# Kernel tuning notes

Hardware: AMD Instinct MI355X
Metric: run time of the kernel (lower is better)

Reference implementation:

```python
import jax, jax.numpy as jnp
import numpy as np

RADIUS = 0.2
NSAMPLE = 32
GROUPS = 4
EPS = 1e-5


def group_norm(x, gamma, beta):
    # x: [B, C, *spatial]; normalize per (batch, group) over channels-in-group + spatial
    B, C = x.shape[0], x.shape[1]
    rest = x.shape[2:]
    xr = x.reshape(B, GROUPS, -1)
    mean = xr.mean(-1, keepdims=True)
    var = xr.var(-1, keepdims=True)
    xr = (xr - mean) * jax.lax.rsqrt(var + EPS)
    x = xr.reshape((B, C) + rest)
    bshape = (1, C) + (1,) * len(rest)
    return x * gamma.reshape(bshape) + beta.reshape(bshape)


def ball_query(pos_t):
    # pos_t: [B, N, 3] -> idx [B, N, NSAMPLE] (query points == all points)
    N = pos_t.shape[1]
    sq = jnp.sum(pos_t * pos_t, axis=-1)  # [B, N]
    d = sq[:, :, None] + sq[:, None, :] - 2.0 * jnp.einsum('bnc,bmc->bnm', pos_t, pos_t)
    ar = jnp.arange(N, dtype=jnp.int32)
    gi = jnp.where(d > RADIUS * RADIUS, N, ar[None, None, :])  # [B, S, N]
    gi = jnp.sort(gi, axis=-1)[:, :, :NSAMPLE]  # ascending in-ball indices first
    first = gi[:, :, :1]
    gi = jnp.where(gi == N, first, gi)  # pad with first neighbor
    return gi


def setup_inputs() -> dict:
    key = jax.random.key(0)
    ks = jax.random.split(key, 6)
    B, C, N = 2, 64, 4096
    M = 4 * C  # mid channels
    return {
        'x': jax.random.normal(ks[0], (B, C, N), jnp.float32),
        'pos': jax.random.uniform(ks[1], (B, 3, N), jnp.float32),
        'w1': jax.random.normal(ks[2], (M, C), jnp.float32) * 0.05,
        'b1': jnp.zeros((M,), jnp.float32),
        'g1': jnp.ones((M,), jnp.float32),
        'be1': jnp.zeros((M,), jnp.float32),
        'wd': 1.0 + jax.random.normal(ks[3], (M,), jnp.float32) * 0.05,
        'gd': jnp.ones((M,), jnp.float32),
        'bed': jnp.zeros((M,), jnp.float32),
        'w2': jax.random.normal(ks[4], (C, M), jnp.float32) * 0.05,
        'b2': jnp.zeros((C,), jnp.float32),
        'g2': jnp.ones((C,), jnp.float32),
        'be2': jnp.zeros((C,), jnp.float32),
    }


def reference(x, pos, w1, b1, g1, be1, wd, gd, bed, w2, b2, g2, be2):
    # x: [B, C, N], pos: [B, 3, N]
    pos_t = jnp.transpose(pos, (0, 2, 1))  # [B, N, 3]
    idx = ball_query(pos_t)  # [B, N, K]

    # conv1 (1x1) -> GroupNorm -> GELU
    h = jnp.einsum('mc,bcn->bmn', w1, x) + b1[None, :, None]
    h = jax.nn.gelu(group_norm(h, g1, be1), approximate=False)  # [B, M, N]

    # gather neighbors: feats [B, N, M] indexed by idx [B, N, K]
    feats = jnp.transpose(h, (0, 2, 1))
    grouped = jax.vmap(lambda f, i: f[i])(feats, idx)  # [B, N, K, M]
    grouped = jnp.transpose(grouped, (0, 3, 1, 2))  # [B, M, N, K]

    # depthwise 1x1 conv (per-channel scale, no bias) -> GroupNorm -> max-pool over K -> GELU
    grouped = grouped * wd[None, :, None, None]
    grouped = group_norm(grouped, gd, bed)
    h2 = jax.nn.gelu(jnp.max(grouped, axis=-1), approximate=False)  # [B, M, N]

    # conv2 (1x1) -> GroupNorm -> residual
    out = jnp.einsum('cm,bmn->bcn', w2, h2) + b2[None, :, None]
    out = group_norm(out, g2, be2)
    return out + x
```

## Files before the change

### kernel.cpp

```cpp
#include <hip/hip_runtime.h>
#include <hip/hip_fp16.h>
#include <math.h>

#define BB 2
#define CC 64
#define NN 4096
#define MM 256
#define KK 32
#define GG 4
#define EPSF 1e-5f

__device__ __forceinline__ float gelu_exact(float x) {
    return 0.5f * x * (1.0f + erff(x * 0.70710678118654752f));
}

__device__ __forceinline__ unsigned pkmax(unsigned a, unsigned b) {
    unsigned d;
    asm volatile("v_pk_max_f16 %0, %1, %2" : "=v"(d) : "v"(a), "v"(b));
    return d;
}
__device__ __forceinline__ unsigned pkmin(unsigned a, unsigned b) {
    unsigned d;
    asm volatile("v_pk_min_f16 %0, %1, %2" : "=v"(d) : "v"(a), "v"(b));
    return d;
}
__device__ __forceinline__ unsigned selpair(unsigned mx, unsigned mn, float g0, float g1) {
    unsigned lo = (g0 >= 0.f) ? (mx & 0x0000FFFFu) : (mn & 0x0000FFFFu);
    unsigned hi = (g1 >= 0.f) ? (mx & 0xFFFF0000u) : (mn & 0xFFFF0000u);
    return lo | hi;
}
__device__ __forceinline__ float bcast_lane(float v, int lane) {
    return __int_as_float(__builtin_amdgcn_readlane(__float_as_int(v), lane));
}

__global__ void k_mlp1(const float* __restrict__ x, const float* __restrict__ w1,
                       const float* __restrict__ b1, float* __restrict__ h,
                       float2* __restrict__ Mp) {
    __shared__ float xs[64 * 128];
    __shared__ float w1t[64 * 32];
    __shared__ float r1[4], r2[4];

    int bx = blockIdx.x;
    int nt = bx & 31, mt = (bx >> 5) & 7, b = bx >> 8;
    int n0 = nt * 128, m0 = mt * 32;
    int t = threadIdx.x;

    {
        int nq = t & 31, ch = t >> 5;
        #pragma unroll
        for (int p = 0; p < 8; p++) {
            int c = p * 8 + ch;
            float4 v = *(const float4*)&x[((size_t)(b * CC + c)) * NN + n0 + nq * 4];
            *(float4*)&xs[c * 128 + nq * 4] = v;
        }
    }
    {
        #pragma unroll
        for (int p = 0; p < 2; p++) {
            int idx = p * 256 + t;
            int m = idx >> 4, cq = idx & 15;
            float4 v = *(const float4*)&w1[(m0 + m) * CC + cq * 4];
            w1t[(cq * 4 + 0) * 32 + m] = v.x;
            w1t[(cq * 4 + 1) * 32 + m] = v.y;
            w1t[(cq * 4 + 2) * 32 + m] = v.z;
            w1t[(cq * 4 + 3) * 32 + m] = v.w;
        }
    }
    __syncthreads();

    int nq = t & 31;
    int mseg = t >> 5;
    float o[4][4];
    #pragma unroll
    for (int i = 0; i < 4; i++)
        #pragma unroll
        for (int j = 0; j < 4; j++) o[i][j] = 0.f;

    for (int c = 0; c < 64; c++) {
        float4 xv = *(float4*)&xs[c * 128 + nq * 4];
        float4 wv = *(float4*)&w1t[c * 32 + mseg * 4];
        o[0][0] = fmaf(wv.x, xv.x, o[0][0]); o[0][1] = fmaf(wv.x, xv.y, o[0][1]);
        o[0][2] = fmaf(wv.x, xv.z, o[0][2]); o[0][3] = fmaf(wv.x, xv.w, o[0][3]);
        o[1][0] = fmaf(wv.y, xv.x, o[1][0]); o[1][1] = fmaf(wv.y, xv.y, o[1][1]);
        o[1][2] = fmaf(wv.y, xv.z, o[1][2]); o[1][3] = fmaf(wv.y, xv.w, o[1][3]);
        o[2][0] = fmaf(wv.z, xv.x, o[2][0]); o[2][1] = fmaf(wv.z, xv.y, o[2][1]);
        o[2][2] = fmaf(wv.z, xv.z, o[2][2]); o[2][3] = fmaf(wv.z, xv.w, o[2][3]);
        o[3][0] = fmaf(wv.w, xv.x, o[3][0]); o[3][1] = fmaf(wv.w, xv.y, o[3][1]);
        o[3][2] = fmaf(wv.w, xv.z, o[3][2]); o[3][3] = fmaf(wv.w, xv.w, o[3][3]);
    }

    float s1 = 0.f, s2 = 0.f;
    #pragma unroll
    for (int mi = 0; mi < 4; mi++) {
        int m = m0 + mseg * 4 + mi;
        float bv = b1[m];
        float4 r;
        r.x = o[mi][0] + bv; r.y = o[mi][1] + bv;
        r.z = o[mi][2] + bv; r.w = o[mi][3] + bv;
        *(float4*)&h[((size_t)(b * MM + m)) * NN + n0 + nq * 4] = r;
        s1 += r.x + r.y + r.z + r.w;
        s2 = fmaf(r.x, r.x, s2); s2 = fmaf(r.y, r.y, s2);
        s2 = fmaf(r.z, r.z, s2); s2 = fmaf(r.w, r.w, s2);
    }
    for (int off = 32; off; off >>= 1) {
        s1 += __shfl_down(s1, off, 64);
        s2 += __shfl_down(s2, off, 64);
    }
    int w = t >> 6, l = t & 63;
    if (l == 0) { r1[w] = s1; r2[w] = s2; }
    __syncthreads();
    if (t == 0) {
        Mp[bx] = make_float2(r1[0] + r1[1] + r1[2] + r1[3],
                             r2[0] + r2[1] + r2[2] + r2[3]);
    }
}

__global__ void k_gn1t_ballq(const float* __restrict__ h, const float* __restrict__ g1,
                             const float* __restrict__ be1, const float* __restrict__ wd,
                             const float2* __restrict__ Mp, __half* __restrict__ pH,
                             float* __restrict__ R,
                             const float* __restrict__ pos, int* __restrict__ idx) {
    __shared__ float tile[64 * 65];
    __shared__ float mv[2];
    int t = threadIdx.x;

    if (blockIdx.x < 512) {
        int id = blockIdx.x;
        int n0 = (id & 63) * 64;
        int g  = (id >> 6) & 3;
        int b  = id >> 8;
        int m0 = g * 64;

        if (t < 64) {
            float2 p2 = Mp[b * 256 + g * 64 + t];
            float s1 = p2.x, s2 = p2.y;
            for (int off = 32; off; off >>= 1) {
                s1 += __shfl_down(s1, off, 64);
                s2 += __shfl_down(s2, off, 64);
            }
            if (t == 0) {
                const double cnt = 64.0 * 4096.0;
                double md = (double)s1 / cnt;
                double vd = (double)s2 / cnt - md * md;
                mv[0] = (float)md;
                mv[1] = rsqrtf((float)vd + EPSF);
            }
        }
        __syncthreads();
        float mean = mv[0], rstd = mv[1];

        int nq = t & 15, mr = t >> 4;
        #pragma unroll
        for (int pp = 0; pp < 4; pp++) {
            int row = pp * 16 + mr;
            int m = m0 + row;
            float a = rstd * g1[m];
            float cc2 = be1[m] - mean * a;
            float wdm = wd[m];
            float4 hv = *(const float4*)&h[((size_t)(b * MM + m)) * NN + n0 + nq * 4];
            tile[row * 65 + nq * 4 + 0] = gelu_exact(fmaf(hv.x, a, cc2)) * wdm;
            tile[row * 65 + nq * 4 + 1] = gelu_exact(fmaf(hv.y, a, cc2)) * wdm;
            tile[row * 65 + nq * 4 + 2] = gelu_exact(fmaf(hv.z, a, cc2)) * wdm;
            tile[row * 65 + nq * 4 + 3] = gelu_exact(fmaf(hv.w, a, cc2)) * wdm;
        }
        __syncthreads();
        #pragma unroll
        for (int pp = 0; pp < 4; pp++) {
            int id2 = pp * 256 + t;
            int nl = id2 >> 4, mq = id2 & 15;
            float a0 = tile[(mq * 4 + 0) * 65 + nl];
            float a1 = tile[(mq * 4 + 1) * 65 + nl];
            float a2 = tile[(mq * 4 + 2) * 65 + nl];
            float a3 = tile[(mq * 4 + 3) * 65 + nl];
            __half2 hA = __float22half2_rn(make_float2(a0, a1));
            __half2 hB = __float22half2_rn(make_float2(a2, a3));
            uint2 st8;
            st8.x = *(unsigned*)&hA; st8.y = *(unsigned*)&hB;
            *(uint2*)((char*)pH + ((((size_t)(b * NN) + n0 + nl)) << 9) + (m0 + mq * 4) * 2) = st8;
            float2 fa = __half22float2(hA);
            float2 fb = __half22float2(hB);
            float t1 = fa.x + fa.y + fb.x + fb.y;
            float t2 = fa.x * fa.x + fa.y * fa.y + fb.x * fb.x + fb.y * fb.y;
            #pragma unroll
            for (int off = 8; off; off >>= 1) {
                t1 += __shfl_down(t1, off, 16);
                t2 += __shfl_down(t2, off, 16);
            }
            if ((t & 15) == 0) {
                float* rr = &R[((size_t)(b * NN) + n0 + nl) * 8];
                rr[g]     = t1;
                rr[4 + g] = t2;
            }
        }
    } else {
        int bx = blockIdx.x - 512;
        int wid  = bx * 4 + (threadIdx.x >> 6);
        int lane = threadIdx.x & 63;
        int b = wid >> 12;
        int n = wid & 4095;
        const float* px = pos + b * 3 * NN;
        const float* py = px + NN;
        const float* pz = py + NN;
        float qx = px[n], qy = py[n], qz = pz[n];
        float qsq = qx*qx + qy*qy + qz*qz;
        int* row = idx + (b * NN + n) * KK;

        int found = 0;
        int first = -1;
        const float R2 = 0.04f;
        for (int m0 = 0; m0 < NN && found < KK; m0 += 64) {
            int m = m0 + lane;
            float ax = px[m], ay = py[m], az = pz[m];
            float msq = ax*ax + ay*ay + az*az;
            float dot = qx*ax + qy*ay + qz*az;
            float d = qsq + msq - 2.0f * dot;
            bool hit = !(d > R2);
            unsigned long long mask = __ballot(hit);
            if (first < 0 && mask) first = m0 + (__ffsll((long long)mask) - 1);
            unsigned long long lt = (lane == 0) ? 0ULL : (mask & ((1ULL << lane) - 1ULL));
            int posh = __popcll(lt);
            if (hit && (found + posh) < KK) row[found + posh] = m;
            found += __popcll(mask);
            if (found > KK) found = KK;
        }
        if (lane < KK && lane >= found) row[lane] = first;
    }
}

__global__ __launch_bounds__(256)
void k_qgather_gstats(const __half* __restrict__ pH, const int* __restrict__ idx,
                      const float* __restrict__ R, const float* __restrict__ gd,
                      __half* __restrict__ pselH, float* __restrict__ Gp) {
    __shared__ float sAcc[8][8];
    int t = threadIdx.x;

    if (blockIdx.x < 2048) {
        int w = t >> 6, l = t & 63;
        int gn = blockIdx.x * 4 + w;
        int b = gn >> 12;

        int hh = l >> 5, cl = l & 31;
        int myidx = idx[gn * KK + cl];
        const char* pb = (const char*)(pH + (size_t)b * NN * 256);
        int laneoff = cl * 16;

        unsigned vmax0 = 0xFC00FC00u, vmax1 = 0xFC00FC00u, vmax2 = 0xFC00FC00u, vmax3 = 0xFC00FC00u;
        unsigned vmin0 = 0x7C007C00u, vmin1 = 0x7C007C00u, vmin2 = 0x7C007C00u, vmin3 = 0x7C007C00u;

        #pragma unroll
        for (int k = 0; k < 16; k++) {
            int ja = __shfl(myidx, 2 * k, 64);
            int jb = __shfl(myidx, 2 * k + 1, 64);
            int j = hh ? jb : ja;
            uint4 raw = *(const uint4*)(pb + (((size_t)j) << 9) + laneoff);
            vmax0 = pkmax(vmax0, raw.x); vmin0 = pkmin(vmin0, raw.x);
            vmax1 = pkmax(vmax1, raw.y); vmin1 = pkmin(vmin1, raw.y);
            vmax2 = pkmax(vmax2, raw.z); vmin2 = pkmin(vmin2, raw.z);
            vmax3 = pkmax(vmax3, raw.w); vmin3 = pkmin(vmin3, raw.w);
        }
        vmax0 = pkmax(vmax0, (unsigned)__shfl_xor((int)vmax0, 32, 64));
        vmax1 = pkmax(vmax1, (unsigned)__shfl_xor((int)vmax1, 32, 64));
        vmax2 = pkmax(vmax2, (unsigned)__shfl_xor((int)vmax2, 32, 64));
        vmax3 = pkmax(vmax3, (unsigned)__shfl_xor((int)vmax3, 32, 64));
        vmin0 = pkmin(vmin0, (unsigned)__shfl_xor((int)vmin0, 32, 64));
        vmin1 = pkmin(vmin1, (unsigned)__shfl_xor((int)vmin1, 32, 64));
        vmin2 = pkmin(vmin2, (unsigned)__shfl_xor((int)vmin2, 32, 64));
        vmin3 = pkmin(vmin3, (unsigned)__shfl_xor((int)vmin3, 32, 64));

        if (hh == 0) {
            const float4* g4 = (const float4*)gd;
            float4 gA = g4[cl * 2], gB = g4[cl * 2 + 1];
            uint4 out;
            out.x = selpair(vmax0, vmin0, gA.x, gA.y);
            out.y = selpair(vmax1, vmin1, gA.z, gA.w);
            out.z = selpair(vmax2, vmin2, gB.x, gB.y);
            out.w = selpair(vmax3, vmin3, gB.z, gB.w);
            *(uint4*)((char*)pselH + (((size_t)gn) << 9) + laneoff) = out;
        }
    } else {
        int bid = blockIdx.x - 2048;
        int hw = t >> 5, cl = t & 31;
        int pbase = bid * 32;
        int b = pbase >> 12;
        float s[8];
        #pragma unroll
        for (int c = 0; c < 8; c++) s[c] = 0.f;
        #pragma unroll
        for (int it = 0; it < 4; it++) {
            int pt = pbase + it * 8 + hw;
            int j = idx[pt * KK + cl];
            const float* rr = &R[((size_t)(b * NN) + j) * 8];
            float4 ra = *(const float4*)rr;
            float4 rb = *(const float4*)(rr + 4);
            s[0] += ra.x; s[1] += ra.y; s[2] += ra.z; s[3] += ra.w;
            s[4] += rb.x; s[5] += rb.y; s[6] += rb.z; s[7] += rb.w;
        }
        #pragma unroll
        for (int off = 16; off; off >>= 1) {
            #pragma unroll
            for (int c = 0; c < 8; c++) s[c] += __shfl_down(s[c], off, 32);
        }
        if (cl == 0) {
            #pragma unroll
            for (int c = 0; c < 8; c++) sAcc[hw][c] = s[c];
        }
        __syncthreads();
        if (t < 8) {
            float v = 0.f;
            #pragma unroll
            for (int k = 0; k < 8; k++) v += sAcc[k][t];
            Gp[bid * 8 + t] = v;
        }
    }
}

__global__ __launch_bounds__(256, 4)
void k_mlp2(const __half* __restrict__ pselH, const float* __restrict__ Gp,
            const float* __restrict__ w2, const float* __restrict__ b2,
            const float* __restrict__ gd, const float* __restrict__ bed,
            float* __restrict__ oraw, float* __restrict__ Op) {
    __shared__ float w2s[64 * 257];
    __shared__ float sw[4][8];
    __shared__ float sA[4][4], sB[4][4];

    int t = threadIdx.x;
    int w = t >> 6, l = t & 63;
    int b  = blockIdx.x >> 7;
    int n0 = (blockIdx.x & 127) * 32 + w * 8;

    #pragma unroll
    for (int p = 0; p < 16; p++) {
        int i = p * 256 + t;
        int c = i >> 6, mq = i & 63;
        float4 v = ((const float4*)w2)[i];
        float* dst = &w2s[c * 257 + mq * 4];
        dst[0] = v.x; dst[1] = v.y; dst[2] = v.z; dst[3] = v.w;
    }

    {
        float s[8] = {0.f, 0.f, 0.f, 0.f, 0.f, 0.f, 0.f, 0.f};
        if (t < 128) {
            const float4* gp = (const float4*)(Gp + ((size_t)(b * 128 + t)) * 8);
            float4 ra = gp[0], rb = gp[1];
            s[0] = ra.x; s[1] = ra.y; s[2] = ra.z; s[3] = ra.w;
            s[4] = rb.x; s[5] = rb.y; s[6] = rb.z; s[7] = rb.w;
        }
        #pragma unroll
        for (int off = 32; off; off >>= 1) {
            #pragma unroll
            for (int c = 0; c < 8; c++) s[c] += __shfl_down(s[c], off, 64);
        }
        if (l == 0) {
            #pragma unroll
            for (int c = 0; c < 8; c++) sw[w][c] = s[c];
        }
    }
    __syncthreads();

    int g = l >> 4;
    double s1 = (double)sw[0][g] + sw[1][g] + sw[2][g] + sw[3][g];
    double s2 = (double)sw[0][4 + g] + sw[1][4 + g] + sw[2][4 + g] + sw[3][4 + g];
    const double cnt2 = 64.0 * 4096.0 * 32.0;
    double m_ = s1 / cnt2;
    double v_ = s2 / cnt2 - m_ * m_;
    float mean = (float)m_;
    float rstd = rsqrtf((float)v_ + EPSF);
    float4 gd4  = ((const float4*)gd)[l];
    float4 bed4 = ((const float4*)bed)[l];
    float ax = rstd * gd4.x, ay = rstd * gd4.y, az = rstd * gd4.z, aw = rstd * gd4.w;
    float cx = bed4.x - mean * ax, cy = bed4.y - mean * ay;
    float cz = bed4.z - mean * az, cw = bed4.w - mean * aw;

    float4 h2r[8];
    #pragma unroll
    for (int j = 0; j < 8; j++) {
        uint2 raw = *(const uint2*)((const char*)pselH +
                     ((((size_t)(b * NN)) + n0 + j) << 9) + l * 8);
        float2 fa = __half22float2(*(__half2*)&raw.x);
        float2 fb = __half22float2(*(__half2*)&raw.y);
        h2r[j].x = gelu_exact(fmaf(fa.x, ax, cx));
        h2r[j].y = gelu_exact(fmaf(fa.y, ay, cy));
        h2r[j].z = gelu_exact(fmaf(fb.x, az, cz));
        h2r[j].w = gelu_exact(fmaf(fb.y, aw, cw));
    }

    const float* w2l = &w2s[l * 257];
    float acc[8];
    #pragma unroll
    for (int j = 0; j < 8; j++) acc[j] = 0.f;

    #pragma unroll 8
    for (int mq = 0; mq < 64; mq++) {
        float w0  = w2l[4 * mq + 0];
        float w1_ = w2l[4 * mq + 1];
        float w2_ = w2l[4 * mq + 2];
        float w3_ = w2l[4 * mq + 3];
        #pragma unroll
        for (int j = 0; j < 8; j++) {
            acc[j] = fmaf(w0,  bcast_lane(h2r[j].x, mq), acc[j]);
            acc[j] = fmaf(w1_, bcast_lane(h2r[j].y, mq), acc[j]);
            acc[j] = fmaf(w2_, bcast_lane(h2r[j].z, mq), acc[j]);
            acc[j] = fmaf(w3_, bcast_lane(h2r[j].w, mq), acc[j]);
        }
    }

    float bias = b2[l];
    float so1 = 0.f, so2 = 0.f;
    #pragma unroll
    for (int j = 0; j < 8; j++) {
        acc[j] += bias;
        so1 += acc[j];
        so2 = fmaf(acc[j], acc[j], so2);
    }
    float* dst = &oraw[((size_t)(b * CC) + l) * NN + n0];
    *(float4*)&dst[0] = make_float4(acc[0], acc[1], acc[2], acc[3]);
    *(float4*)&dst[4] = make_float4(acc[4], acc[5], acc[6], acc[7]);

    so1 += __shfl_down(so1, 8, 16); so2 += __shfl_down(so2, 8, 16);
    so1 += __shfl_down(so1, 4, 16); so2 += __shfl_down(so2, 4, 16);
    so1 += __shfl_down(so1, 2, 16); so2 += __shfl_down(so2, 2, 16);
    so1 += __shfl_down(so1, 1, 16); so2 += __shfl_down(so2, 1, 16);
    if ((l & 15) == 0) { sA[w][l >> 4] = so1; sB[w][l >> 4] = so2; }
    __syncthreads();
    if (t < 8) {
        int is2 = t >> 2, gg = t & 3;
        float v = is2 ? (sB[0][gg] + sB[1][gg] + sB[2][gg] + sB[3][gg])
                      : (sA[0][gg] + sA[1][gg] + sA[2][gg] + sA[3][gg]);
        Op[blockIdx.x * 8 + t] = v;
    }
}

__global__ void k_final(const float* __restrict__ oraw, const float* __restrict__ x,
                        const float* __restrict__ g2, const float* __restrict__ be2,
                        const float* __restrict__ Op, float* __restrict__ out) {
    __shared__ float fw[4][8];
    int t = threadIdx.x;
    int i4 = blockIdx.x * 256 + t;
    int base = i4 * 4;
    int b = base >> 18;

    {
        float s[8] = {0.f, 0.f, 0.f, 0.f, 0.f, 0.f, 0.f, 0.f};
        if (t < 128) {
            const float4* rp = (const float4*)(Op + ((size_t)(b * 128 + t)) * 8);
            float4 ra = rp[0], rb = rp[1];
            s[0] = ra.x; s[1] = ra.y; s[2] = ra.z; s[3] = ra.w;
            s[4] = rb.x; s[5] = rb.y; s[6] = rb.z; s[7] = rb.w;
        }
        #pragma unroll
        for (int off = 32; off; off >>= 1) {
            #pragma unroll
            for (int c = 0; c < 8; c++) s[c] += __shfl_down(s[c], off, 64);
        }
        if ((t & 63) == 0) {
            #pragma unroll
            for (int c = 0; c < 8; c++) fw[t >> 6][c] = s[c];
        }
    }
    __syncthreads();

    int c = (base >> 12) & 63;
    int g = c >> 4;
    double s1 = (double)fw[0][g] + fw[1][g] + fw[2][g] + fw[3][g];
    double s2 = (double)fw[0][4 + g] + fw[1][4 + g] + fw[2][4 + g] + fw[3][4 + g];
    const double cnt = 16.0 * 4096.0;
    double mean_d = s1 / cnt;
    double var_d  = s2 / cnt - mean_d * mean_d;
    float mean = (float)mean_d;
    float rstd = rsqrtf((float)var_d + EPSF);
    float sc = rstd * g2[c];
    float ad = be2[c] - mean * sc;
    float4 o = ((const float4*)oraw)[i4];
    float4 xv = ((const float4*)x)[i4];
    float4 r;
    r.x = fmaf(o.x, sc, ad) + xv.x;
    r.y = fmaf(o.y, sc, ad) + xv.y;
    r.z = fmaf(o.z, sc, ad) + xv.z;
    r.w = fmaf(o.w, sc, ad) + xv.w;
    ((float4*)out)[i4] = r;
}

extern "C" void kernel_launch(void* const* d_in, const int* in_sizes, int n_in,
                              void* d_out, int out_size, void* d_ws, size_t ws_size,
                              hipStream_t stream) {
    const float* x   = (const float*)d_in[0];
    const float* pos = (const float*)d_in[1];
    const float* w1  = (const float*)d_in[2];
    const float* b1  = (const float*)d_in[3];
    const float* g1  = (const float*)d_in[4];
    const float* be1 = (const float*)d_in[5];
    const float* wd  = (const float*)d_in[6];
    const float* gd  = (const float*)d_in[7];
    const float* bed = (const float*)d_in[8];
    const float* w2  = (const float*)d_in[9];
    const float* b2  = (const float*)d_in[10];
    const float* g2  = (const float*)d_in[11];
    const float* be2 = (const float*)d_in[12];
    float* out = (float*)d_out;

    char* wsb = (char*)d_ws;
    float*  h     = (float*)wsb;
    __half* pH    = (__half*)(wsb + 8388608);
    __half* pselH = (__half*)(wsb + 12582912);
    float*  oraw  = (float*)(wsb + 16777216);
    int*    idx   = (int*)(wsb + 18874368);
    float*  R     = (float*)(wsb + 19922944);
    float2* Mp    = (float2*)(wsb + 20185088);
    float*  Gp    = (float*)(wsb + 20189184);
    float*  Op    = (float*)(wsb + 20197376);

    k_mlp1<<<512, 256, 0, stream>>>(x, w1, b1, h, Mp);
    k_gn1t_ballq<<<2560, 256, 0, stream>>>(h, g1, be1, wd, Mp, pH, R, pos, idx);
    k_qgather_gstats<<<2304, 256, 0, stream>>>(pH, idx, R, gd, pselH, Gp);
    k_mlp2<<<256, 256, 0, stream>>>(pselH, Gp, w2, b2, gd, bed, oraw, Op);
    k_final<<<512, 256, 0, stream>>>(oraw, x, g2, be2, Op, out);
}
```

Before: 148.9 us.

## Move ball query into mlp1 kernel and fuse final GN into mlp2 via grid barrier

```diff
diff --git a/kernel.cpp b/kernel.cpp
--- a/kernel.cpp
+++ b/kernel.cpp
@@ -33,164 +33,87 @@
     return __int_as_float(__builtin_amdgcn_readlane(__float_as_int(v), lane));
 }
 
-__global__ void k_mlp1(const float* __restrict__ x, const float* __restrict__ w1,
-                       const float* __restrict__ b1, float* __restrict__ h,
-                       float2* __restrict__ Mp) {
+__global__ void k_mlp1_ballq(const float* __restrict__ x, const float* __restrict__ w1,
+                             const float* __restrict__ b1, float* __restrict__ h,
+                             float2* __restrict__ Mp,
+                             const float* __restrict__ pos, int* __restrict__ idx) {
     __shared__ float xs[64 * 128];
     __shared__ float w1t[64 * 32];
     __shared__ float r1[4], r2[4];
-
-    int bx = blockIdx.x;
-    int nt = bx & 31, mt = (bx >> 5) & 7, b = bx >> 8;
-    int n0 = nt * 128, m0 = mt * 32;
     int t = threadIdx.x;
 
-    {
-        int nq = t & 31, ch = t >> 5;
-        #pragma unroll
-        for (int p = 0; p < 8; p++) {
-            int c = p * 8 + ch;
-            float4 v = *(const float4*)&x[((size_t)(b * CC + c)) * NN + n0 + nq * 4];
-            *(float4*)&xs[c * 128 + nq * 4] = v;
-        }
-    }
-    {
-        #pragma unroll
-        for (int p = 0; p < 2; p++) {
-            int idx = p * 256 + t;
-            int m = idx >> 4, cq = idx & 15;
-            float4 v = *(const float4*)&w1[(m0 + m) * CC + cq * 4];
-            w1t[(cq * 4 + 0) * 32 + m] = v.x;
-            w1t[(cq * 4 + 1) * 32 + m] = v.y;
-            w1t[(cq * 4 + 2) * 32 + m] = v.z;
-            w1t[(cq * 4 + 3) * 32 + m] = v.w;
-        }
-    }
-    __syncthreads();
-
-    int nq = t & 31;
-    int mseg = t >> 5;
-    float o[4][4];
-    #pragma unroll
-    for (int i = 0; i < 4; i++)
-        #pragma unroll
-        for (int j = 0; j < 4; j++) o[i][j] = 0.f;
-
-    for (int c = 0; c < 64; c++) {
-        float4 xv = *(float4*)&xs[c * 128 + nq * 4];
-        float4 wv = *(float4*)&w1t[c * 32 + mseg * 4];
-        o[0][0] = fmaf(wv.x, xv.x, o[0][0]); o[0][1] = fmaf(wv.x, xv.y, o[0][1]);
-        o[0][2] = fmaf(wv.x, xv.z, o[0][2]); o[0][3] = fmaf(wv.x, xv.w, o[0][3]);
-        o[1][0] = fmaf(wv.y, xv.x, o[1][0]); o[1][1] = fmaf(wv.y, xv.y, o[1][1]);
-        o[1][2] = fmaf(wv.y, xv.z, o[1][2]); o[1][3] = fmaf(wv.y, xv.w, o[1][3]);
-        o[2][0] = fmaf(wv.z, xv.x, o[2][0]); o[2][1] = fmaf(wv.z, xv.y, o[2][1]);
-        o[2][2] = fmaf(wv.z, xv.z, o[2][2]); o[2][3] = fmaf(wv.z, xv.w, o[2][3]);
-        o[3][0] = fmaf(wv.w, xv.x, o[3][0]); o[3][1] = fmaf(wv.w, xv.y, o[3][1]);
-        o[3][2] = fmaf(wv.w, xv.z, o[3][2]); o[3][3] = fmaf(wv.w, xv.w, o[3][3]);
-    }
-
-    float s1 = 0.f, s2 = 0.f;
-    #pragma unroll
-    for (int mi = 0; mi < 4; mi++) {
-        int m = m0 + mseg * 4 + mi;
-        float bv = b1[m];
-        float4 r;
-        r.x = o[mi][0] + bv; r.y = o[mi][1] + bv;
-        r.z = o[mi][2] + bv; r.w = o[mi][3] + bv;
-        *(float4*)&h[((size_t)(b * MM + m)) * NN + n0 + nq * 4] = r;
-        s1 += r.x + r.y + r.z + r.w;
-        s2 = fmaf(r.x, r.x, s2); s2 = fmaf(r.y, r.y, s2);
-        s2 = fmaf(r.z, r.z, s2); s2 = fmaf(r.w, r.w, s2);
-    }
-    for (int off = 32; off; off >>= 1) {
-        s1 += __shfl_down(s1, off, 64);
-        s2 += __shfl_down(s2, off, 64);
-    }
-    int w = t >> 6, l = t & 63;
-    if (l == 0) { r1[w] = s1; r2[w] = s2; }
-    __syncthreads();
-    if (t == 0) {
-        Mp[bx] = make_float2(r1[0] + r1[1] + r1[2] + r1[3],
-                             r2[0] + r2[1] + r2[2] + r2[3]);
-    }
-}
-
-__global__ void k_gn1t_ballq(const float* __restrict__ h, const float* __restrict__ g1,
-                             const float* __restrict__ be1, const float* __restrict__ wd,
-                             const float2* __restrict__ Mp, __half* __restrict__ pH,
-                             float* __restrict__ R,
-                             const float* __restrict__ pos, int* __restrict__ idx) {
-    __shared__ float tile[64 * 65];
-    __shared__ float mv[2];
-    int t = threadIdx.x;
-
     if (blockIdx.x < 512) {
-        int id = blockIdx.x;
-        int n0 = (id & 63) * 64;
-        int g  = (id >> 6) & 3;
-        int b  = id >> 8;
-        int m0 = g * 64;
-
-        if (t < 64) {
-            float2 p2 = Mp[b * 256 + g * 64 + t];
-            float s1 = p2.x, s2 = p2.y;
-            for (int off = 32; off; off >>= 1) {
-                s1 += __shfl_down(s1, off, 64);
-                s2 += __shfl_down(s2, off, 64);
+        int bx = blockIdx.x;
+        int nt = bx & 31, mt = (bx >> 5) & 7, b = bx >> 8;
+        int n0 = nt * 128, m0 = mt * 32;
+
+        {
+            int nq = t & 31, ch = t >> 5;
+            #pragma unroll
+            for (int p = 0; p < 8; p++) {
+                int c = p * 8 + ch;
+                float4 v = *(const float4*)&x[((size_t)(b * CC + c)) * NN + n0 + nq * 4];
+                *(float4*)&xs[c * 128 + nq * 4] = v;
             }
-            if (t == 0) {
-                const double cnt = 64.0 * 4096.0;
-                double md = (double)s1 / cnt;
-                double vd = (double)s2 / cnt - md * md;
-                mv[0] = (float)md;
-                mv[1] = rsqrtf((float)vd + EPSF);
+        }
+        {
+            #pragma unroll
+            for (int p = 0; p < 2; p++) {
+                int i = p * 256 + t;
+                int m = i >> 4, cq = i & 15;
+                float4 v = *(const float4*)&w1[(m0 + m) * CC + cq * 4];
+                w1t[(cq * 4 + 0) * 32 + m] = v.x;
+                w1t[(cq * 4 + 1) * 32 + m] = v.y;
+                w1t[(cq * 4 + 2) * 32 + m] = v.z;
+                w1t[(cq * 4 + 3) * 32 + m] = v.w;
             }
         }
         __syncthreads();
-        float mean = mv[0], rstd = mv[1];
-
-        int nq = t & 15, mr = t >> 4;
-        #pragma unroll
-        for (int pp = 0; pp < 4; pp++) {
-            int row = pp * 16 + mr;
-            int m = m0 + row;
-            float a = rstd * g1[m];
-            float cc2 = be1[m] - mean * a;
-            float wdm = wd[m];
-            float4 hv = *(const float4*)&h[((size_t)(b * MM + m)) * NN + n0 + nq * 4];
-            tile[row * 65 + nq * 4 + 0] = gelu_exact(fmaf(hv.x, a, cc2)) * wdm;
-            tile[row * 65 + nq * 4 + 1] = gelu_exact(fmaf(hv.y, a, cc2)) * wdm;
-            tile[row * 65 + nq * 4 + 2] = gelu_exact(fmaf(hv.z, a, cc2)) * wdm;
-            tile[row * 65 + nq * 4 + 3] = gelu_exact(fmaf(hv.w, a, cc2)) * wdm;
-        }
+
+        int nq = t & 31;
+        int mseg = t >> 5;
+        float o[4][4];
+        #pragma unroll
+        for (int i = 0; i < 4; i++)
+            #pragma unroll
+            for (int j = 0; j < 4; j++) o[i][j] = 0.f;
+
+        for (int c = 0; c < 64; c++) {
+            float4 xv = *(float4*)&xs[c * 128 + nq * 4];
+            float4 wv = *(float4*)&w1t[c * 32 + mseg * 4];
+            o[0][0] = fmaf(wv.x, xv.x, o[0][0]); o[0][1] = fmaf(wv.x, xv.y, o[0][1]);
+            o[0][2] = fmaf(wv.x, xv.z, o[0][2]); o[0][3] = fmaf(wv.x, xv.w, o[0][3]);
+            o[1][0] = fmaf(wv.y, xv.x, o[1][0]); o[1][1] = fmaf(wv.y, xv.y, o[1][1]);
+            o[1][2] = fmaf(wv.y, xv.z, o[1][2]); o[1][3] = fmaf(wv.y, xv.w, o[1][3]);
+            o[2][0] = fmaf(wv.z, xv.x, o[2][0]); o[2][1] = fmaf(wv.z, xv.y, o[2][1]);
+            o[2][2] = fmaf(wv.z, xv.z, o[2][2]); o[2][3] = fmaf(wv.z, xv.w, o[2][3]);
+            o[3][0] = fmaf(wv.w, xv.x, o[3][0]); o[3][1] = fmaf(wv.w, xv.y, o[3][1]);
+            o[3][2] = fmaf(wv.w, xv.z, o[3][2]); o[3][3] = fmaf(wv.w, xv.w, o[3][3]);
+        }
+
+        float s1 = 0.f, s2 = 0.f;
+        #pragma unroll
+        for (int mi = 0; mi < 4; mi++) {
+            int m = m0 + mseg * 4 + mi;
+            float bv = b1[m];
+            float4 r;
+            r.x = o[mi][0] + bv; r.y = o[mi][1] + bv;
+            r.z = o[mi][2] + bv; r.w = o[mi][3] + bv;
+            *(float4*)&h[((size_t)(b * MM + m)) * NN + n0 + nq * 4] = r;
+            s1 += r.x + r.y + r.z + r.w;
+            s2 = fmaf(r.x, r.x, s2); s2 = fmaf(r.y, r.y, s2);
+            s2 = fmaf(r.z, r.z, s2); s2 = fmaf(r.w, r.w, s2);
+        }
+        for (int off = 32; off; off >>= 1) {
+            s1 += __shfl_down(s1, off, 64);
+            s2 += __shfl_down(s2, off, 64);
+        }
+        int w = t >> 6, l = t & 63;
+        if (l == 0) { r1[w] = s1; r2[w] = s2; }
         __syncthreads();
-        #pragma unroll
-        for (int pp = 0; pp < 4; pp++) {
-            int id2 = pp * 256 + t;
-            int nl = id2 >> 4, mq = id2 & 15;
-            float a0 = tile[(mq * 4 + 0) * 65 + nl];
-            float a1 = tile[(mq * 4 + 1) * 65 + nl];
-            float a2 = tile[(mq * 4 + 2) * 65 + nl];
-            float a3 = tile[(mq * 4 + 3) * 65 + nl];
-            __half2 hA = __float22half2_rn(make_float2(a0, a1));
-            __half2 hB = __float22half2_rn(make_float2(a2, a3));
-            uint2 st8;
-            st8.x = *(unsigned*)&hA; st8.y = *(unsigned*)&hB;
-            *(uint2*)((char*)pH + ((((size_t)(b * NN) + n0 + nl)) << 9) + (m0 + mq * 4) * 2) = st8;
-            float2 fa = __half22float2(hA);
-            float2 fb = __half22float2(hB);
-            float t1 = fa.x + fa.y + fb.x + fb.y;
-            float t2 = fa.x * fa.x + fa.y * fa.y + fb.x * fb.x + fb.y * fb.y;
-            #pragma unroll
-            for (int off = 8; off; off >>= 1) {
-                t1 += __shfl_down(t1, off, 16);
-                t2 += __shfl_down(t2, off, 16);
-            }
-            if ((t & 15) == 0) {
-                float* rr = &R[((size_t)(b * NN) + n0 + nl) * 8];
-                rr[g]     = t1;
-                rr[4 + g] = t2;
-            }
+        if (t == 0) {
+            Mp[bx] = make_float2(r1[0] + r1[1] + r1[2] + r1[3],
+                                 r2[0] + r2[1] + r2[2] + r2[3]);
         }
     } else {
         int bx = blockIdx.x - 512;
@@ -227,6 +150,84 @@
     }
 }
 
+__global__ void k_gn1t(const float* __restrict__ h, const float* __restrict__ g1,
+                       const float* __restrict__ be1, const float* __restrict__ wd,
+                       const float2* __restrict__ Mp, __half* __restrict__ pH,
+                       float* __restrict__ R, unsigned* __restrict__ bar) {
+    __shared__ float tile[64 * 65];
+    __shared__ float mv[2];
+    int t = threadIdx.x;
+    if (blockIdx.x == 0 && t == 0) *bar = 0u;
+
+    int id = blockIdx.x;
+    int n0 = (id & 63) * 64;
+    int g  = (id >> 6) & 3;
+    int b  = id >> 8;
+    int m0 = g * 64;
+
+    if (t < 64) {
+        float2 p2 = Mp[b * 256 + g * 64 + t];
+        float s1 = p2.x, s2 = p2.y;
+        for (int off = 32; off; off >>= 1) {
+            s1 += __shfl_down(s1, off, 64);
+            s2 += __shfl_down(s2, off, 64);
+        }
+        if (t == 0) {
+            const double cnt = 64.0 * 4096.0;
+            double md = (double)s1 / cnt;
+            double vd = (double)s2 / cnt - md * md;
+            mv[0] = (float)md;
+            mv[1] = rsqrtf((float)vd + EPSF);
+        }
+    }
+    __syncthreads();
+    float mean = mv[0], rstd = mv[1];
+
+    int nq = t & 15, mr = t >> 4;
+    #pragma unroll
+    for (int pp = 0; pp < 4; pp++) {
+        int row = pp * 16 + mr;
+        int m = m0 + row;
+        float a = rstd * g1[m];
+        float cc2 = be1[m] - mean * a;
+        float wdm = wd[m];
+        float4 hv = *(const float4*)&h[((size_t)(b * MM + m)) * NN + n0 + nq * 4];
+        tile[row * 65 + nq * 4 + 0] = gelu_exact(fmaf(hv.x, a, cc2)) * wdm;
+        tile[row * 65 + nq * 4 + 1] = gelu_exact(fmaf(hv.y, a, cc2)) * wdm;
+        tile[row * 65 + nq * 4 + 2] = gelu_exact(fmaf(hv.z, a, cc2)) * wdm;
+        tile[row * 65 + nq * 4 + 3] = gelu_exact(fmaf(hv.w, a, cc2)) * wdm;
+    }
+    __syncthreads();
+    #pragma unroll
+    for (int pp = 0; pp < 4; pp++) {
+        int id2 = pp * 256 + t;
+        int nl = id2 >> 4, mq = id2 & 15;
+        float a0 = tile[(mq * 4 + 0) * 65 + nl];
+        float a1 = tile[(mq * 4 + 1) * 65 + nl];
+        float a2 = tile[(mq * 4 + 2) * 65 + nl];
+        float a3 = tile[(mq * 4 + 3) * 65 + nl];
+        __half2 hA = __float22half2_rn(make_float2(a0, a1));
+        __half2 hB = __float22half2_rn(make_float2(a2, a3));
+        uint2 st8;
+        st8.x = *(unsigned*)&hA; st8.y = *(unsigned*)&hB;
+        *(uint2*)((char*)pH + ((((size_t)(b * NN) + n0 + nl)) << 9) + (m0 + mq * 4) * 2) = st8;
+        float2 fa = __half22float2(hA);
+        float2 fb = __half22float2(hB);
+        float t1 = fa.x + fa.y + fb.x + fb.y;
+        float t2 = fa.x * fa.x + fa.y * fa.y + fb.x * fb.x + fb.y * fb.y;
+        #pragma unroll
+        for (int off = 8; off; off >>= 1) {
+            t1 += __shfl_down(t1, off, 16);
+            t2 += __shfl_down(t2, off, 16);
+        }
+        if ((t & 15) == 0) {
+            float* rr = &R[((size_t)(b * NN) + n0 + nl) * 8];
+            rr[g]     = t1;
+            rr[4 + g] = t2;
+        }
+    }
+}
+
 __global__ __launch_bounds__(256)
 void k_qgather_gstats(const __half* __restrict__ pH, const int* __restrict__ idx,
                       const float* __restrict__ R, const float* __restrict__ gd,
@@ -270,12 +271,12 @@
         if (hh == 0) {
             const float4* g4 = (const float4*)gd;
             float4 gA = g4[cl * 2], gB = g4[cl * 2 + 1];
-            uint4 out;
-            out.x = selpair(vmax0, vmin0, gA.x, gA.y);
-            out.y = selpair(vmax1, vmin1, gA.z, gA.w);
-            out.z = selpair(vmax2, vmin2, gB.x, gB.y);
-            out.w = selpair(vmax3, vmin3, gB.z, gB.w);
-            *(uint4*)((char*)pselH + (((size_t)gn) << 9) + laneoff) = out;
+            uint4 o4;
+            o4.x = selpair(vmax0, vmin0, gA.x, gA.y);
+            o4.y = selpair(vmax1, vmin1, gA.z, gA.w);
+            o4.z = selpair(vmax2, vmin2, gB.x, gB.y);
+            o4.w = selpair(vmax3, vmin3, gB.z, gB.w);
+            *(uint4*)((char*)pselH + (((size_t)gn) << 9) + laneoff) = o4;
         }
     } else {
         int bid = blockIdx.x - 2048;
@@ -315,13 +316,17 @@
 }
 
 __global__ __launch_bounds__(256, 4)
-void k_mlp2(const __half* __restrict__ pselH, const float* __restrict__ Gp,
-            const float* __restrict__ w2, const float* __restrict__ b2,
-            const float* __restrict__ gd, const float* __restrict__ bed,
-            float* __restrict__ oraw, float* __restrict__ Op) {
+void k_mlp2f(const __half* __restrict__ pselH, const float* __restrict__ Gp,
+             const float* __restrict__ w2, const float* __restrict__ b2,
+             const float* __restrict__ gd, const float* __restrict__ bed,
+             float* __restrict__ oraw, float* __restrict__ Op,
+             unsigned* bar,
+             const float* __restrict__ x, const float* __restrict__ g2,
+             const float* __restrict__ be2, float* __restrict__ out) {
     __shared__ float w2s[64 * 257];
     __shared__ float sw[4][8];
     __shared__ float sA[4][4], sB[4][4];
+    __shared__ float fw[4][8];
 
     int t = threadIdx.x;
     int w = t >> 6, l = t & 63;
@@ -428,56 +433,65 @@
                       : (sA[0][gg] + sA[1][gg] + sA[2][gg] + sA[3][gg]);
         Op[blockIdx.x * 8 + t] = v;
     }
-}
-
-__global__ void k_final(const float* __restrict__ oraw, const float* __restrict__ x,
-                        const float* __restrict__ g2, const float* __restrict__ be2,
-                        const float* __restrict__ Op, float* __restrict__ out) {
-    __shared__ float fw[4][8];
-    int t = threadIdx.x;
-    int i4 = blockIdx.x * 256 + t;
-    int base = i4 * 4;
-    int b = base >> 18;
-
-    {
-        float s[8] = {0.f, 0.f, 0.f, 0.f, 0.f, 0.f, 0.f, 0.f};
-        if (t < 128) {
-            const float4* rp = (const float4*)(Op + ((size_t)(b * 128 + t)) * 8);
-            float4 ra = rp[0], rb = rp[1];
-            s[0] = ra.x; s[1] = ra.y; s[2] = ra.z; s[3] = ra.w;
-            s[4] = rb.x; s[5] = rb.y; s[6] = rb.z; s[7] = rb.w;
-        }
-        #pragma unroll
-        for (int off = 32; off; off >>= 1) {
-            #pragma unroll
-            for (int c = 0; c < 8; c++) s[c] += __shfl_down(s[c], off, 64);
-        }
-        if ((t & 63) == 0) {
-            #pragma unroll
-            for (int c = 0; c < 8; c++) fw[t >> 6][c] = s[c];
-        }
-    }
+
     __syncthreads();
-
-    int c = (base >> 12) & 63;
-    int g = c >> 4;
-    double s1 = (double)fw[0][g] + fw[1][g] + fw[2][g] + fw[3][g];
-    double s2 = (double)fw[0][4 + g] + fw[1][4 + g] + fw[2][4 + g] + fw[3][4 + g];
-    const double cnt = 16.0 * 4096.0;
-    double mean_d = s1 / cnt;
-    double var_d  = s2 / cnt - mean_d * mean_d;
-    float mean = (float)mean_d;
-    float rstd = rsqrtf((float)var_d + EPSF);
-    float sc = rstd * g2[c];
-    float ad = be2[c] - mean * sc;
-    float4 o = ((const float4*)oraw)[i4];
-    float4 xv = ((const float4*)x)[i4];
-    float4 r;
-    r.x = fmaf(o.x, sc, ad) + xv.x;
-    r.y = fmaf(o.y, sc, ad) + xv.y;
-    r.z = fmaf(o.z, sc, ad) + xv.z;
-    r.w = fmaf(o.w, sc, ad) + xv.w;
-    ((float4*)out)[i4] = r;
+    __threadfence();
+    if (t == 0) {
+        __hip_atomic_fetch_add(bar, 1u, __ATOMIC_RELEASE, __HIP_MEMORY_SCOPE_AGENT);
+        while (__hip_atomic_load(bar, __ATOMIC_ACQUIRE, __HIP_MEMORY_SCOPE_AGENT) < 256u) {
+            __builtin_amdgcn_s_sleep(16);
+        }
+    }
+    __syncthreads();
+    __threadfence();
+
+    for (int q = 0; q < 2; q++) {
+        int fb = blockIdx.x * 2 + q;
+        int i4 = fb * 256 + t;
+        int base = i4 * 4;
+        int fbat = base >> 18;
+
+        __syncthreads();
+        {
+            float s[8] = {0.f, 0.f, 0.f, 0.f, 0.f, 0.f, 0.f, 0.f};
+            if (t < 128) {
+                const float4* rp = (const float4*)(Op + ((size_t)(fbat * 128 + t)) * 8);
+                float4 ra = rp[0], rb = rp[1];
+                s[0] = ra.x; s[1] = ra.y; s[2] = ra.z; s[3] = ra.w;
+                s[4] = rb.x; s[5] = rb.y; s[6] = rb.z; s[7] = rb.w;
+            }
+            #pragma unroll
+            for (int off = 32; off; off >>= 1) {
+                #pragma unroll
+                for (int c = 0; c < 8; c++) s[c] += __shfl_down(s[c], off, 64);
+            }
+            if ((t & 63) == 0) {
+                #pragma unroll
+                for (int c = 0; c < 8; c++) fw[t >> 6][c] = s[c];
+            }
+        }
+        __syncthreads();
+
+        int c = (base >> 12) & 63;
+        int gf = c >> 4;
+        double f1 = (double)fw[0][gf] + fw[1][gf] + fw[2][gf] + fw[3][gf];
+        double f2 = (double)fw[0][4 + gf] + fw[1][4 + gf] + fw[2][4 + gf] + fw[3][4 + gf];
+        const double cntf = 16.0 * 4096.0;
+        double mean_d = f1 / cntf;
+        double var_d  = f2 / cntf - mean_d * mean_d;
+        float meanf = (float)mean_d;
+        float rstdf = rsqrtf((float)var_d + EPSF);
+        float sc = rstdf * g2[c];
+        float ad = be2[c] - meanf * sc;
+        float4 o = ((const float4*)oraw)[i4];
+        float4 xv = ((const float4*)x)[i4];
+        float4 r;
+        r.x = fmaf(o.x, sc, ad) + xv.x;
+        r.y = fmaf(o.y, sc, ad) + xv.y;
+        r.z = fmaf(o.z, sc, ad) + xv.z;
+        r.w = fmaf(o.w, sc, ad) + xv.w;
+        ((float4*)out)[i4] = r;
+    }
 }
 
 extern "C" void kernel_launch(void* const* d_in, const int* in_sizes, int n_in,
@@ -499,19 +513,20 @@
     float* out = (float*)d_out;
 
     char* wsb = (char*)d_ws;
-    float*  h     = (float*)wsb;
-    __half* pH    = (__half*)(wsb + 8388608);
-    __half* pselH = (__half*)(wsb + 12582912);
-    float*  oraw  = (float*)(wsb + 16777216);
-    int*    idx   = (int*)(wsb + 18874368);
-    float*  R     = (float*)(wsb + 19922944);
-    float2* Mp    = (float2*)(wsb + 20185088);
-    float*  Gp    = (float*)(wsb + 20189184);
-    float*  Op    = (float*)(wsb + 20197376);
-
-    k_mlp1<<<512, 256, 0, stream>>>(x, w1, b1, h, Mp);
-    k_gn1t_ballq<<<2560, 256, 0, stream>>>(h, g1, be1, wd, Mp, pH, R, pos, idx);
+    float*    h     = (float*)wsb;
+    __half*   pH    = (__half*)(wsb + 8388608);
+    __half*   pselH = (__half*)(wsb + 12582912);
+    float*    oraw  = (float*)(wsb + 16777216);
+    int*      idx   = (int*)(wsb + 18874368);
+    float*    R     = (float*)(wsb + 19922944);
+    float2*   Mp    = (float2*)(wsb + 20185088);
+    float*    Gp    = (float*)(wsb + 20189184);
+    float*    Op    = (float*)(wsb + 20197376);
+    unsigned* bar   = (unsigned*)(wsb + 20205568);
+
+    k_mlp1_ballq<<<2560, 256, 0, stream>>>(x, w1, b1, h, Mp, pos, idx);
+    k_gn1t<<<512, 256, 0, stream>>>(h, g1, be1, wd, Mp, pH, R, bar);
     k_qgather_gstats<<<2304, 256, 0, stream>>>(pH, idx, R, gd, pselH, Gp);
-    k_mlp2<<<256, 256, 0, stream>>>(pselH, Gp, w2, b2, gd, bed, oraw, Op);
-    k_final<<<512, 256, 0, stream>>>(oraw, x, g2, be2, Op, out);
-}
+    k_mlp2f<<<256, 256, 0, stream>>>(pselH, Gp, w2, b2, gd, bed, oraw, Op, bar,
+                                     x, g2, be2, out);
+}
```

New measurement: 225.8 us. 1.52x slower.
